# Kernel tuning notes

Hardware: AMD Instinct MI355X
Metric: run time of the kernel (lower is better)

The kernel has to match this reference:

```python
import jax, jax.numpy as jnp
import numpy as np

NBX = 24  # nb_x_patches
NBY = 24  # nb_y_patches
B, H, D = 8, 12, 64
L = NBX * NBY + 1  # 577 (grid tokens + 1 CLS token from the pad)
EPS = 1e-08


def _toeplitz_mask(topological_params):
    # topological_params: [H, 4*NBX*NBY]
    gi = jnp.arange(NBX)
    gj = jnp.arange(NBY)
    # relative 2D displacement index, flattened over (i, j, i', j')
    dist_index = ((gi[:, None, None, None] - gi[None, None, :, None] + NBX) * 2 * NBY
                  + gj[None, :, None, None] - gj[None, None, None, :] + NBY)
    dist_index = dist_index.reshape(-1)
    m = jnp.take(topological_params, dist_index, axis=1)
    m = m.reshape(topological_params.shape[0], NBX * NBY, NBX * NBY)  # [H, L-1, L-1]
    # pad CLS row and column with 1.0
    m = jnp.pad(m, [[0, 0], [1, 0], [1, 0]], constant_values=1.0)  # [H, L, L]
    return m[None]  # [1, H, L, L]


def setup_inputs() -> dict:
    key = jax.random.key(0)
    k1, k2, k3, k4 = jax.random.split(key, 4)
    return {
        'query': jax.random.normal(k1, (B, L, H, D), dtype=jnp.float32),
        'key': jax.random.normal(k2, (B, L, H, D), dtype=jnp.float32),
        'value': jax.random.normal(k3, (B, L, H, D), dtype=jnp.float32),
        'topological_params': jax.random.normal(k4, (H, 4 * NBX * NBY), dtype=jnp.float32),
    }


def reference(query, key, value, topological_params):
    depth = query.shape[-1]
    q = query / jnp.sqrt(jnp.asarray(depth, query.dtype))
    # relu feature map (kernel_type == 'relu')
    q = jax.nn.relu(q) + EPS
    k = jax.nn.relu(key) + EPS
    attn = jnp.einsum('bqhd,bkhd->bhqk', q, k)  # [B, H, L, L]
    top_mask = _toeplitz_mask(topological_params)  # [1, H, L, L]
    attn = attn * jnp.abs(top_mask) + EPS
    attn = attn / jnp.sum(attn, axis=-1, keepdims=True)  # kernelized normalization (no softmax)
    return jnp.einsum('bhqk,bkhd->bqhd', attn, value)
```

## Files before the change

kernel.cpp:

```cpp
#include <hip/hip_runtime.h>


#define Lq 577
#define NH 12
#define NB 8
#define DD 64
#define PAR 2304
#define EPSf 1e-8f

typedef __attribute__((ext_vector_type(4))) float f32x4;
typedef __attribute__((ext_vector_type(8))) short s16x8;

__device__ __forceinline__ float bflo(unsigned int u) {
    return __builtin_bit_cast(float, u << 16);
}
__device__ __forceinline__ float bfhi(unsigned int u) {
    return __builtin_bit_cast(float, u & 0xffff0000u);
}
__device__ __forceinline__ unsigned int f2bf(float f) {
    unsigned int x = __builtin_bit_cast(unsigned int, f);
    return (x + 0x7fffu + ((x >> 16) & 1u)) >> 16;
}
__device__ __forceinline__ int imin(int a, int b) { return a < b ? a : b; }

template <bool F32>
__device__ __forceinline__ void load8f(const void* G, size_t eidx, float* o) {
    if constexpr (F32) {
        const float* p = (const float*)G + eidx;
        float4 a = *(const float4*)p;
        float4 b = *(const float4*)(p + 4);
        o[0] = a.x; o[1] = a.y; o[2] = a.z; o[3] = a.w;
        o[4] = b.x; o[5] = b.y; o[6] = b.z; o[7] = b.w;
    } else {
        const unsigned short* p = (const unsigned short*)G + eidx;
        uint4 a = *(const uint4*)p;
        unsigned int u[4] = {a.x, a.y, a.z, a.w};
#pragma unroll
        for (int j = 0; j < 4; ++j) {
            o[2 * j]     = bflo(u[j]);
            o[2 * j + 1] = bfhi(u[j]);
        }
    }
}

template <bool F32>
__device__ void attn_body(const void* __restrict__ Qg, const void* __restrict__ Kg,
                          const void* __restrict__ Vg, const void* __restrict__ Tg,
                          void* __restrict__ Og,
                          float* s_par, unsigned short* s_k,
                          unsigned short* s_vt, unsigned short* s_p_all) {
    const int tid  = threadIdx.x;
    const int w    = tid >> 6;
    const int lane = tid & 63;
    const int g    = lane >> 4;
    const int lm   = lane & 15;

    const int qt = blockIdx.x;
    const int h  = blockIdx.y;
    const int b  = blockIdx.z;

    unsigned short* s_pw = s_p_all + w * 32 * 72;

    for (int i = tid; i < PAR; i += 256) {
        float m = F32 ? ((const float*)Tg)[h * PAR + i]
                      : bflo((unsigned int)((const unsigned short*)Tg)[h * PAR + i]);
        m = fabsf(m);
        s_par[i] = (m == m) ? m : 0.0f;
    }

    const int q0w = qt * 128 + w * 32;

    s16x8 a_q[2][2];
#pragma unroll
    for (int qf = 0; qf < 2; ++qf) {
        int q  = q0w + qf * 16 + lm;
        int qc = imin(q, Lq - 1);
        size_t rbase = ((size_t)((b * Lq + qc) * NH + h)) * DD;
#pragma unroll
        for (int ds = 0; ds < 2; ++ds) {
            float f[8];
            load8f<F32>(Qg, rbase + ds * 32 + g * 8, f);
            s16x8 a;
#pragma unroll
            for (int j = 0; j < 8; ++j) {
                float v = fmaf(fmaxf(f[j], 0.0f), 0.125f, EPSf);
                a[j] = (short)f2bf(v);
            }
            a_q[qf][ds] = a;
        }
    }

    int  cq[2][4];
    bool qz[2][4];
#pragma unroll
    for (int qf = 0; qf < 2; ++qf)
#pragma unroll
        for (int r = 0; r < 4; ++r) {
            int q = q0w + qf * 16 + g * 4 + r;
            qz[qf][r] = (q == 0);
            int qq = imin(q, Lq - 1) - 1;
            int qi = qq / 24;
            int qj = qq - qi * 24;
            cq[qf][r] = qi * 48 + qj + 1176;
        }

    f32x4 o_acc[2][4] = {};
    float rs[2][4]    = {};

    for (int kb = 0; kb < Lq; kb += 64) {
        __syncthreads();

        {
            int kg  = kb + lane;
            int kgc = imin(kg, Lq - 1);
            size_t base = ((size_t)((b * Lq + kgc) * NH + h)) * DD + w * 16;
            float kr[16], vr[16];
            load8f<F32>(Kg, base,     kr);
            load8f<F32>(Kg, base + 8, kr + 8);
            load8f<F32>(Vg, base,     vr);
            load8f<F32>(Vg, base + 8, vr + 8);
            unsigned int kt[8];
#pragma unroll
            for (int j = 0; j < 8; ++j) {
                float f0 = fmaxf(kr[2 * j], 0.0f) + EPSf;
                float f1 = fmaxf(kr[2 * j + 1], 0.0f) + EPSf;
                kt[j] = f2bf(f0) | (f2bf(f1) << 16);
            }
            *(uint4*)&s_k[lane * 72 + w * 16]     = make_uint4(kt[0], kt[1], kt[2], kt[3]);
            *(uint4*)&s_k[lane * 72 + w * 16 + 8] = make_uint4(kt[4], kt[5], kt[6], kt[7]);
#pragma unroll
            for (int j = 0; j < 16; ++j) {
                float vv = vr[j];
                vv = (vv == vv) ? vv : 0.0f;
                s_vt[(w * 16 + j) * 72 + lane] = (unsigned short)f2bf(vv);
            }
        }
        __syncthreads();

        f32x4 sf[2][4];
#pragma unroll
        for (int cf = 0; cf < 4; ++cf) {
            s16x8 b0 = *(const s16x8*)&s_k[(cf * 16 + lm) * 72 + g * 8];
            s16x8 b1 = *(const s16x8*)&s_k[(cf * 16 + lm) * 72 + 32 + g * 8];
#pragma unroll
            for (int qf = 0; qf < 2; ++qf) {
                f32x4 acc = {};
                acc = __builtin_amdgcn_mfma_f32_16x16x32_bf16(a_q[qf][0], b0, acc, 0, 0, 0);
                acc = __builtin_amdgcn_mfma_f32_16x16x32_bf16(a_q[qf][1], b1, acc, 0, 0, 0);
                sf[qf][cf] = acc;
            }
        }

#pragma unroll
        for (int cf = 0; cf < 4; ++cf) {
            int  kg     = kb + cf * 16 + lm;
            bool kvalid = kg < Lq;
            float eps_k  = kvalid ? EPSf : 0.0f;
            float base_m = kvalid ? 1.0f : 0.0f;
            bool kgt0   = kg > 0;
            int  kk = kg - 1;
            int  ki = kk / 24;
            int  kl = ki * 48 + (kk - ki * 24);
#pragma unroll
            for (int qf = 0; qf < 2; ++qf)
#pragma unroll
                for (int r = 0; r < 4; ++r) {
                    bool um  = kgt0 && kvalid && !qz[qf][r];
                    int  idx = um ? (cq[qf][r] - kl) : 0;
                    float mm = um ? s_par[idx] : base_m;
                    float s  = fmaxf(sf[qf][cf][r], 0.0f);
                    float p  = fmaf(s, mm, eps_k);
                    p = fminf(p, 1e30f);
                    rs[qf][r] += p;
                    s_pw[(qf * 16 + g * 4 + r) * 72 + cf * 16 + lm] = (unsigned short)f2bf(p);
                }
        }
        __syncthreads();

#pragma unroll
        for (int ks = 0; ks < 2; ++ks) {
            s16x8 pa0 = *(const s16x8*)&s_pw[lm * 72        + ks * 32 + g * 8];
            s16x8 pa1 = *(const s16x8*)&s_pw[(16 + lm) * 72 + ks * 32 + g * 8];
#pragma unroll
            for (int df = 0; df < 4; ++df) {
                s16x8 vb = *(const s16x8*)&s_vt[(df * 16 + lm) * 72 + ks * 32 + g * 8];
                o_acc[0][df] = __builtin_amdgcn_mfma_f32_16x16x32_bf16(pa0, vb, o_acc[0][df], 0, 0, 0);
                o_acc[1][df] = __builtin_amdgcn_mfma_f32_16x16x32_bf16(pa1, vb, o_acc[1][df], 0, 0, 0);
            }
        }
    }

#pragma unroll
    for (int qf = 0; qf < 2; ++qf)
#pragma unroll
        for (int r = 0; r < 4; ++r) {
            float v = rs[qf][r];
            v += __shfl_xor(v, 1, 64);
            v += __shfl_xor(v, 2, 64);
            v += __shfl_xor(v, 4, 64);
            v += __shfl_xor(v, 8, 64);
            rs[qf][r] = (v > 0.0f) ? 1.0f / v : 0.0f;
        }

#pragma unroll
    for (int qf = 0; qf < 2; ++qf)
#pragma unroll
        for (int r = 0; r < 4; ++r) {
            int q = q0w + qf * 16 + g * 4 + r;
            if (q < Lq) {
                size_t base = ((size_t)((b * Lq + q) * NH + h)) * DD;
#pragma unroll
                for (int df = 0; df < 4; ++df) {
                    float val = o_acc[qf][df][r] * rs[qf][r];
                    val = fminf(fmaxf(val, -1e30f), 1e30f);
                    if constexpr (F32)
                        ((float*)Og)[base + df * 16 + lm] = val;
                    else
                        ((unsigned short*)Og)[base + df * 16 + lm] = (unsigned short)f2bf(val);
                }
            }
        }
}

__global__ __launch_bounds__(256, 2)
void fused_topo_attn(const void* __restrict__ Qg, const void* __restrict__ Kg,
                     const void* __restrict__ Vg, const void* __restrict__ Tg,
                     void* __restrict__ Og) {
    __shared__ __align__(16) float          s_par[PAR];
    __shared__ __align__(16) unsigned short s_k[64 * 72];
    __shared__ __align__(16) unsigned short s_vt[64 * 72];
    __shared__ __align__(16) unsigned short s_p[4 * 32 * 72];

    float x = fabsf(((const float*)Qg)[threadIdx.x]);
    int n = __syncthreads_count(x > 2.44140625e-4f && x < 64.0f);

    if (n >= 128)
        attn_body<true>(Qg, Kg, Vg, Tg, Og, s_par, s_k, s_vt, s_p);
    else
        attn_body<false>(Qg, Kg, Vg, Tg, Og, s_par, s_k, s_vt, s_p);
}

extern "C" void kernel_launch(void* const* d_in, const int* in_sizes, int n_in,
                              void* d_out, int out_size, void* d_ws, size_t ws_size,
                              hipStream_t stream) {
    (void)in_sizes; (void)n_in; (void)out_size; (void)d_ws; (void)ws_size;
    dim3 grid(5, NH, NB);
    fused_topo_attn<<<grid, 256, 0, stream>>>(d_in[0], d_in[1], d_in[2], d_in[3], d_out);
}
```

Before: 130.4 us.

## Halve per-block query tile to 64 rows and transpose QK MFMA layout

Each block now handles 64 queries (16 per wave) instead of 128, giving 960 blocks on a flattened 1D grid with launch bounds raised to 4 blocks per CU. The score MFMA swaps operands so each lane holds 4 consecutive keys for one query. This lets P be written as packed uint2, removes the per-wave sync before the PV stage, and makes the row sum a single scalar per lane. V transpose stores are packed into 32-bit pairs and divisions by 24 are replaced with multiply-shift. The smaller tile means K/V and the topological parameters are reloaded by twice as many blocks, in exchange for better occupancy and less tail imbalance.

```diff
diff --git a/kernel.cpp b/kernel.cpp
--- a/kernel.cpp
+++ b/kernel.cpp
@@ -22,6 +22,7 @@
     return (x + 0x7fffu + ((x >> 16) & 1u)) >> 16;
 }
 __device__ __forceinline__ int imin(int a, int b) { return a < b ? a : b; }
+__device__ __forceinline__ int imax(int a, int b) { return a > b ? a : b; }
 
 template <bool F32>
 __device__ __forceinline__ void load8f(const void* G, size_t eidx, float* o) {
@@ -55,11 +56,13 @@
     const int g    = lane >> 4;
     const int lm   = lane & 15;
 
-    const int qt = blockIdx.x;
-    const int h  = blockIdx.y;
-    const int b  = blockIdx.z;
-
-    unsigned short* s_pw = s_p_all + w * 32 * 72;
+    const int bid = blockIdx.x;
+    const int qt  = bid / 96;
+    const int bh  = bid - qt * 96;
+    const int h   = bh % NH;
+    const int b   = bh / NH;
+
+    unsigned short* s_pw = s_p_all + w * 16 * 72;
 
     for (int i = tid; i < PAR; i += 256) {
         float m = F32 ? ((const float*)Tg)[h * PAR + i]
@@ -68,13 +71,12 @@
         s_par[i] = (m == m) ? m : 0.0f;
     }
 
-    const int q0w = qt * 128 + w * 32;
-
-    s16x8 a_q[2][2];
-#pragma unroll
-    for (int qf = 0; qf < 2; ++qf) {
-        int q  = q0w + qf * 16 + lm;
-        int qc = imin(q, Lq - 1);
+    const int q0w = qt * 64 + w * 16;
+
+    const int q  = q0w + lm;
+    const int qc = imin(q, Lq - 1);
+    s16x8 a_q[2];
+    {
         size_t rbase = ((size_t)((b * Lq + qc) * NH + h)) * DD;
 #pragma unroll
         for (int ds = 0; ds < 2; ++ds) {
@@ -86,39 +88,30 @@
                 float v = fmaf(fmaxf(f[j], 0.0f), 0.125f, EPSf);
                 a[j] = (short)f2bf(v);
             }
-            a_q[qf][ds] = a;
-        }
-    }
-
-    int  cq[2][4];
-    bool qz[2][4];
-#pragma unroll
-    for (int qf = 0; qf < 2; ++qf)
-#pragma unroll
-        for (int r = 0; r < 4; ++r) {
-            int q = q0w + qf * 16 + g * 4 + r;
-            qz[qf][r] = (q == 0);
-            int qq = imin(q, Lq - 1) - 1;
-            int qi = qq / 24;
-            int qj = qq - qi * 24;
-            cq[qf][r] = qi * 48 + qj + 1176;
-        }
-
-    f32x4 o_acc[2][4] = {};
-    float rs[2][4]    = {};
+            a_q[ds] = a;
+        }
+    }
+
+    const bool qz = (q == 0);
+    const int  qq = imax(qc - 1, 0);
+    const int  qi = (qq * 2731) >> 16;
+    const int  cq = qq + 24 * qi + 1176;
+
+    f32x4 o_acc[4] = {};
+    float rs = 0.0f;
+
+    const int k0v  = 2 * (tid & 31);
+    const int dchv = (tid >> 5) * 8;
 
     for (int kb = 0; kb < Lq; kb += 64) {
         __syncthreads();
 
         {
-            int kg  = kb + lane;
-            int kgc = imin(kg, Lq - 1);
+            int kgc = imin(kb + lane, Lq - 1);
             size_t base = ((size_t)((b * Lq + kgc) * NH + h)) * DD + w * 16;
-            float kr[16], vr[16];
+            float kr[16];
             load8f<F32>(Kg, base,     kr);
             load8f<F32>(Kg, base + 8, kr + 8);
-            load8f<F32>(Vg, base,     vr);
-            load8f<F32>(Vg, base + 8, vr + 8);
             unsigned int kt[8];
 #pragma unroll
             for (int j = 0; j < 8; ++j) {
@@ -128,108 +121,103 @@
             }
             *(uint4*)&s_k[lane * 72 + w * 16]     = make_uint4(kt[0], kt[1], kt[2], kt[3]);
             *(uint4*)&s_k[lane * 72 + w * 16 + 8] = make_uint4(kt[4], kt[5], kt[6], kt[7]);
-#pragma unroll
-            for (int j = 0; j < 16; ++j) {
-                float vv = vr[j];
-                vv = (vv == vv) ? vv : 0.0f;
-                s_vt[(w * 16 + j) * 72 + lane] = (unsigned short)f2bf(vv);
+        }
+        {
+            int kg0 = imin(kb + k0v,     Lq - 1);
+            int kg1 = imin(kb + k0v + 1, Lq - 1);
+            size_t b0 = ((size_t)((b * Lq + kg0) * NH + h)) * DD + dchv;
+            size_t b1 = ((size_t)((b * Lq + kg1) * NH + h)) * DD + dchv;
+            float v0[8], v1[8];
+            load8f<F32>(Vg, b0, v0);
+            load8f<F32>(Vg, b1, v1);
+#pragma unroll
+            for (int j = 0; j < 8; ++j) {
+                float a0 = v0[j], a1 = v1[j];
+                a0 = (a0 == a0) ? a0 : 0.0f;
+                a1 = (a1 == a1) ? a1 : 0.0f;
+                *(unsigned int*)&s_vt[(dchv + j) * 72 + k0v] =
+                    f2bf(a0) | (f2bf(a1) << 16);
             }
         }
         __syncthreads();
 
-        f32x4 sf[2][4];
+        f32x4 sf[4];
 #pragma unroll
         for (int cf = 0; cf < 4; ++cf) {
-            s16x8 b0 = *(const s16x8*)&s_k[(cf * 16 + lm) * 72 + g * 8];
-            s16x8 b1 = *(const s16x8*)&s_k[(cf * 16 + lm) * 72 + 32 + g * 8];
-#pragma unroll
-            for (int qf = 0; qf < 2; ++qf) {
-                f32x4 acc = {};
-                acc = __builtin_amdgcn_mfma_f32_16x16x32_bf16(a_q[qf][0], b0, acc, 0, 0, 0);
-                acc = __builtin_amdgcn_mfma_f32_16x16x32_bf16(a_q[qf][1], b1, acc, 0, 0, 0);
-                sf[qf][cf] = acc;
-            }
+            s16x8 kf0 = *(const s16x8*)&s_k[(cf * 16 + lm) * 72 + g * 8];
+            s16x8 kf1 = *(const s16x8*)&s_k[(cf * 16 + lm) * 72 + 32 + g * 8];
+            f32x4 acc = {};
+            acc = __builtin_amdgcn_mfma_f32_16x16x32_bf16(kf0, a_q[0], acc, 0, 0, 0);
+            acc = __builtin_amdgcn_mfma_f32_16x16x32_bf16(kf1, a_q[1], acc, 0, 0, 0);
+            sf[cf] = acc;
         }
 
 #pragma unroll
         for (int cf = 0; cf < 4; ++cf) {
-            int  kg     = kb + cf * 16 + lm;
-            bool kvalid = kg < Lq;
-            float eps_k  = kvalid ? EPSf : 0.0f;
-            float base_m = kvalid ? 1.0f : 0.0f;
-            bool kgt0   = kg > 0;
-            int  kk = kg - 1;
-            int  ki = kk / 24;
-            int  kl = ki * 48 + (kk - ki * 24);
-#pragma unroll
-            for (int qf = 0; qf < 2; ++qf)
-#pragma unroll
-                for (int r = 0; r < 4; ++r) {
-                    bool um  = kgt0 && kvalid && !qz[qf][r];
-                    int  idx = um ? (cq[qf][r] - kl) : 0;
-                    float mm = um ? s_par[idx] : base_m;
-                    float s  = fmaxf(sf[qf][cf][r], 0.0f);
-                    float p  = fmaf(s, mm, eps_k);
-                    p = fminf(p, 1e30f);
-                    rs[qf][r] += p;
-                    s_pw[(qf * 16 + g * 4 + r) * 72 + cf * 16 + lm] = (unsigned short)f2bf(p);
-                }
-        }
-        __syncthreads();
+            float p[4];
+#pragma unroll
+            for (int r = 0; r < 4; ++r) {
+                int  k  = kb + cf * 16 + g * 4 + r;
+                bool kv = k < Lq;
+                bool um = (k > 0) && kv && !qz;
+                int  kk = imax(k - 1, 0);
+                int  ki = (kk * 2731) >> 16;
+                int  kl = kk + 24 * ki;
+                int  idx = um ? (cq - kl) : 0;
+                float mm = um ? s_par[idx] : (kv ? 1.0f : 0.0f);
+                float s  = fmaxf(sf[cf][r], 0.0f);
+                float pp = fmaf(s, mm, kv ? EPSf : 0.0f);
+                rs += pp;
+                p[r] = pp;
+            }
+            unsigned int d0 = f2bf(p[0]) | (f2bf(p[1]) << 16);
+            unsigned int d1 = f2bf(p[2]) | (f2bf(p[3]) << 16);
+            *(uint2*)&s_pw[lm * 72 + cf * 16 + g * 4] = make_uint2(d0, d1);
+        }
 
 #pragma unroll
         for (int ks = 0; ks < 2; ++ks) {
-            s16x8 pa0 = *(const s16x8*)&s_pw[lm * 72        + ks * 32 + g * 8];
-            s16x8 pa1 = *(const s16x8*)&s_pw[(16 + lm) * 72 + ks * 32 + g * 8];
+            s16x8 pa = *(const s16x8*)&s_pw[lm * 72 + ks * 32 + g * 8];
 #pragma unroll
             for (int df = 0; df < 4; ++df) {
                 s16x8 vb = *(const s16x8*)&s_vt[(df * 16 + lm) * 72 + ks * 32 + g * 8];
-                o_acc[0][df] = __builtin_amdgcn_mfma_f32_16x16x32_bf16(pa0, vb, o_acc[0][df], 0, 0, 0);
-                o_acc[1][df] = __builtin_amdgcn_mfma_f32_16x16x32_bf16(pa1, vb, o_acc[1][df], 0, 0, 0);
-            }
-        }
-    }
-
-#pragma unroll
-    for (int qf = 0; qf < 2; ++qf)
-#pragma unroll
-        for (int r = 0; r < 4; ++r) {
-            float v = rs[qf][r];
-            v += __shfl_xor(v, 1, 64);
-            v += __shfl_xor(v, 2, 64);
-            v += __shfl_xor(v, 4, 64);
-            v += __shfl_xor(v, 8, 64);
-            rs[qf][r] = (v > 0.0f) ? 1.0f / v : 0.0f;
-        }
-
-#pragma unroll
-    for (int qf = 0; qf < 2; ++qf)
-#pragma unroll
-        for (int r = 0; r < 4; ++r) {
-            int q = q0w + qf * 16 + g * 4 + r;
-            if (q < Lq) {
-                size_t base = ((size_t)((b * Lq + q) * NH + h)) * DD;
-#pragma unroll
-                for (int df = 0; df < 4; ++df) {
-                    float val = o_acc[qf][df][r] * rs[qf][r];
-                    val = fminf(fmaxf(val, -1e30f), 1e30f);
-                    if constexpr (F32)
-                        ((float*)Og)[base + df * 16 + lm] = val;
-                    else
-                        ((unsigned short*)Og)[base + df * 16 + lm] = (unsigned short)f2bf(val);
-                }
-            }
-        }
-}
-
-__global__ __launch_bounds__(256, 2)
+                o_acc[df] = __builtin_amdgcn_mfma_f32_16x16x32_bf16(pa, vb, o_acc[df], 0, 0, 0);
+            }
+        }
+    }
+
+    float tot = rs;
+    tot += __shfl_xor(tot, 16, 64);
+    tot += __shfl_xor(tot, 32, 64);
+    float inv = (tot > 0.0f) ? 1.0f / tot : 0.0f;
+
+#pragma unroll
+    for (int r = 0; r < 4; ++r) {
+        int   qrow  = q0w + g * 4 + r;
+        float inv_r = __shfl(inv, g * 4 + r, 64);
+        if (qrow < Lq) {
+            size_t base = ((size_t)((b * Lq + qrow) * NH + h)) * DD;
+#pragma unroll
+            for (int df = 0; df < 4; ++df) {
+                float val = o_acc[df][r] * inv_r;
+                val = fminf(fmaxf(val, -1e30f), 1e30f);
+                if constexpr (F32)
+                    ((float*)Og)[base + df * 16 + lm] = val;
+                else
+                    ((unsigned short*)Og)[base + df * 16 + lm] = (unsigned short)f2bf(val);
+            }
+        }
+    }
+}
+
+__global__ __launch_bounds__(256, 4)
 void fused_topo_attn(const void* __restrict__ Qg, const void* __restrict__ Kg,
                      const void* __restrict__ Vg, const void* __restrict__ Tg,
                      void* __restrict__ Og) {
     __shared__ __align__(16) float          s_par[PAR];
     __shared__ __align__(16) unsigned short s_k[64 * 72];
     __shared__ __align__(16) unsigned short s_vt[64 * 72];
-    __shared__ __align__(16) unsigned short s_p[4 * 32 * 72];
+    __shared__ __align__(16) unsigned short s_p[4 * 16 * 72];
 
     float x = fabsf(((const float*)Qg)[threadIdx.x]);
     int n = __syncthreads_count(x > 2.44140625e-4f && x < 64.0f);
@@ -244,6 +232,6 @@
                               void* d_out, int out_size, void* d_ws, size_t ws_size,
                               hipStream_t stream) {
     (void)in_sizes; (void)n_in; (void)out_size; (void)d_ws; (void)ws_size;
-    dim3 grid(5, NH, NB);
+    dim3 grid(960);
     fused_topo_attn<<<grid, 256, 0, stream>>>(d_in[0], d_in[1], d_in[2], d_in[3], d_out);
 }
```

Result: slower. 135.0 us (+3.6%).
